# Performance work log

Hardware: AMD Instinct MI355X
Metric: run time of the kernel (lower is better)

The kernel has to match this reference:

```python
import jax, jax.numpy as jnp
import numpy as np

HEADS = 8
DIM_HEAD = 64
DIM = 512
HIDDEN = HEADS * DIM_HEAD  # 512


def setup_inputs() -> dict:
    key = jax.random.key(0)
    k1, k2, k3, k4 = jax.random.split(key, 4)
    B, H, W = 8, 64, 64
    x = jax.random.normal(k1, (B, DIM, H, W), dtype=jnp.float32)
    # Conv2d 1x1 weights stored as [out_ch, in_ch] (kernel 1x1 squeezed)
    w_qkv = jax.random.normal(k2, (3 * HIDDEN, DIM), dtype=jnp.float32) * (1.0 / np.sqrt(DIM))
    w_out = jax.random.normal(k3, (DIM, HIDDEN), dtype=jnp.float32) * (1.0 / np.sqrt(HIDDEN))
    b_out = jax.random.normal(k4, (DIM,), dtype=jnp.float32) * 0.01
    return {"x": x, "w_qkv": w_qkv, "w_out": w_out, "b_out": b_out}


def reference(x, w_qkv, w_out, b_out):
    b, c, h, w = x.shape
    n = h * w
    # to_qkv: 1x1 conv == channel GEMM
    qkv = jnp.einsum('bchw,oc->bohw', x, w_qkv)               # [b, 3*heads*dh, h, w]
    qkv = qkv.reshape(b, 3, HEADS, DIM_HEAD, n)               # split (qkv heads c), flatten (h w)
    q, k, v = qkv[:, 0], qkv[:, 1], qkv[:, 2]                 # each [b, heads, dh, n]
    k = jax.nn.softmax(k, axis=-1)                            # softmax over spatial tokens
    context = jnp.einsum('bhdn,bhen->bhde', k, v)             # [b, heads, dh, dh]
    out = jnp.einsum('bhde,bhdn->bhen', context, q)           # [b, heads, dh, n]
    out = out.reshape(b, HIDDEN, h, w)
    # to_out: 1x1 conv with bias
    return jnp.einsum('bchw,oc->bohw', out, w_out) + b_out[None, :, None, None]
```

## Files before the change

kernel.cpp:

```cpp
#include <hip/hip_runtime.h>
#include <hip/hip_bf16.h>


typedef __attribute__((ext_vector_type(8))) __bf16 bf16x8;
typedef __attribute__((ext_vector_type(4))) float f32x4;
typedef __attribute__((ext_vector_type(8))) unsigned short u16x8;

__device__ __forceinline__ unsigned short f2b(float f) {
  unsigned int u = __builtin_bit_cast(unsigned int, f);
  unsigned int r = (u + 0x7FFFu + ((u >> 16) & 1u)) >> 16;
  return (unsigned short)r;
}
__device__ __forceinline__ float b2f(unsigned short h) {
  unsigned int u = ((unsigned int)h) << 16;
  return __builtin_bit_cast(float, u);
}

__global__ __launch_bounds__(256) void prep_wkv_kernel(const float* __restrict__ w,
                                                       unsigned short* __restrict__ wkv) {
  int i = (blockIdx.x * 256 + threadIdx.x) * 4;
  const float* src = w + 512 * 512;
  #pragma unroll
  for (int j = 0; j < 4; ++j) wkv[i + j] = f2b(src[i + j]);
}

__global__ __launch_bounds__(256) void prep_wqT_kernel(const float* __restrict__ w,
                                                       unsigned short* __restrict__ WqT) {
  __shared__ unsigned short tile[64][65];
  const int ct = blockIdx.x, ot = blockIdx.y;
  const int c0 = ct * 64, o0 = ot * 64;
  const int tc = threadIdx.x & 63, tr = threadIdx.x >> 6;
  #pragma unroll
  for (int i = 0; i < 16; ++i) {
    int row = tr * 16 + i;
    tile[tc][row] = f2b(w[(long)(o0 + row) * 512 + c0 + tc]);
  }
  __syncthreads();
  #pragma unroll
  for (int i = 0; i < 16; ++i) {
    int row = tr * 16 + i;
    WqT[(long)(c0 + row) * 512 + o0 + tc] = tile[row][tc];
  }
}

__global__ __launch_bounds__(256) void transpose_x_kernel(const float* __restrict__ x,
                                                          unsigned short* __restrict__ xT) {
  __shared__ unsigned short tile[64][65];
  const int b = blockIdx.z, ct = blockIdx.y, nt = blockIdx.x;
  const int c0 = ct * 64, n0 = nt * 64;
  const int tc = threadIdx.x & 63, tr = threadIdx.x >> 6;
  const float* xp = x + ((long)b * 512 + c0) * 4096 + n0;
  #pragma unroll
  for (int i = 0; i < 16; ++i) {
    int row = tr * 16 + i;
    tile[tc][row] = f2b(xp[(long)row * 4096 + tc]);
  }
  __syncthreads();
  unsigned short* xtp = xT + ((long)b * 4096 + n0) * 512 + c0;
  #pragma unroll
  for (int i = 0; i < 16; ++i) {
    int row = tr * 16 + i;
    xtp[(long)row * 512 + tc] = tile[row][tc];
  }
}

__global__ __launch_bounds__(256) void gemm128_bt(
    const unsigned short* __restrict__ A, long strideA,
    const unsigned short* __restrict__ BT, long strideBT,
    void* __restrict__ Cout, long strideC, int ldc,
    const float* __restrict__ bias) {
  constexpr int K = 512;
  const int b = blockIdx.z;
  const int m0 = blockIdx.y * 128;
  const int n0 = blockIdx.x * 128;
  const unsigned short* Ab = A + (long)b * strideA;
  const unsigned short* Bb = BT + (long)b * strideBT;

  __shared__ unsigned short lds[2 * 128 * 64];
  char* ldsc = (char*)lds;

  const int tid = threadIdx.x;
  const int wave = tid >> 6;
  const int lane = tid & 63;
  const int wr = wave >> 1;
  const int wc = wave & 1;

  f32x4 acc[4][4];
  const f32x4 zero = {0.f, 0.f, 0.f, 0.f};
  #pragma unroll
  for (int i = 0; i < 4; ++i)
    #pragma unroll
    for (int j = 0; j < 4; ++j) acc[i][j] = zero;

  for (int kt = 0; kt < K; kt += 64) {
    #pragma unroll
    for (int q = 0; q < 4; ++q) {
      unsigned base = q * 4096 + wave * 1024;
      unsigned D = base + lane * 16;
      unsigned row = D >> 7;
      unsigned g = (D >> 4) & 7;
      unsigned gl = g ^ (row & 7);
      const unsigned short* srcA = Ab + (long)(m0 + row) * K + kt + gl * 8;
      __builtin_amdgcn_global_load_lds(
          (const __attribute__((address_space(1))) unsigned int*)srcA,
          (__attribute__((address_space(3))) unsigned int*)(ldsc + base), 16, 0, 0);
      const unsigned short* srcB = Bb + (long)(n0 + row) * K + kt + gl * 8;
      __builtin_amdgcn_global_load_lds(
          (const __attribute__((address_space(1))) unsigned int*)srcB,
          (__attribute__((address_space(3))) unsigned int*)(ldsc + 16384 + base), 16, 0, 0);
    }
    __syncthreads();

    bf16x8 af[2][4], bfr[2][4];
    #pragma unroll
    for (int ks = 0; ks < 2; ++ks) {
      #pragma unroll
      for (int mi = 0; mi < 4; ++mi) {
        unsigned row = wr * 64 + mi * 16 + (lane & 15);
        unsigned g = ((unsigned)(ks * 4 + (lane >> 4))) ^ (row & 7);
        af[ks][mi] = *(const bf16x8*)(ldsc + row * 128 + g * 16);
      }
      #pragma unroll
      for (int ni = 0; ni < 4; ++ni) {
        unsigned row = wc * 64 + ni * 16 + (lane & 15);
        unsigned g = ((unsigned)(ks * 4 + (lane >> 4))) ^ (row & 7);
        bfr[ks][ni] = *(const bf16x8*)(ldsc + 16384 + row * 128 + g * 16);
      }
    }
    #pragma unroll
    for (int ks = 0; ks < 2; ++ks)
      #pragma unroll
      for (int mi = 0; mi < 4; ++mi)
        #pragma unroll
        for (int ni = 0; ni < 4; ++ni)
          acc[mi][ni] = __builtin_amdgcn_mfma_f32_16x16x32_bf16(
              af[ks][mi], bfr[ks][ni], acc[mi][ni], 0, 0, 0);
    __syncthreads();
  }

  const int r0 = (lane >> 4) * 4;
  const int cn = lane & 15;
  if (bias != nullptr) {
    float* C = (float*)Cout + (long)b * strideC;
    #pragma unroll
    for (int mi = 0; mi < 4; ++mi) {
      int o = m0 + wr * 64 + mi * 16 + r0;
      #pragma unroll
      for (int ni = 0; ni < 4; ++ni) {
        int n = n0 + wc * 64 + ni * 16 + cn;
        #pragma unroll
        for (int r = 0; r < 4; ++r)
          C[(long)(o + r) * ldc + n] = acc[mi][ni][r] + bias[o + r];
      }
    }
  } else {
    unsigned short* C = (unsigned short*)Cout + (long)b * strideC;
    #pragma unroll
    for (int mi = 0; mi < 4; ++mi) {
      int o = m0 + wr * 64 + mi * 16 + r0;
      #pragma unroll
      for (int ni = 0; ni < 4; ++ni) {
        int n = n0 + wc * 64 + ni * 16 + cn;
        #pragma unroll
        for (int r = 0; r < 4; ++r)
          C[(long)(o + r) * ldc + n] = f2b(acc[mi][ni][r]);
      }
    }
  }
}

__global__ __launch_bounds__(256) void rowstat_kernel(const unsigned short* __restrict__ kv,
                                                      float* __restrict__ stats) {
  const int row = blockIdx.x;
  const int b = row >> 9, d = row & 511;
  const unsigned short* kp = kv + ((long)b * 1024 + d) * 4096;
  const int tid = threadIdx.x, wave = tid >> 6, lane = tid & 63;
  __shared__ float red[8];

  float v[16];
  u16x8 l0 = *(const u16x8*)(kp + tid * 8);
  u16x8 l1 = *(const u16x8*)(kp + 2048 + tid * 8);
  #pragma unroll
  for (int j = 0; j < 8; ++j) { v[j] = b2f(l0[j]); v[8 + j] = b2f(l1[j]); }

  float m = v[0];
  #pragma unroll
  for (int j = 1; j < 16; ++j) m = fmaxf(m, v[j]);
  #pragma unroll
  for (int off = 32; off > 0; off >>= 1) m = fmaxf(m, __shfl_xor(m, off));
  if (lane == 0) red[wave] = m;
  __syncthreads();
  m = fmaxf(fmaxf(red[0], red[1]), fmaxf(red[2], red[3]));

  float s = 0.f;
  #pragma unroll
  for (int j = 0; j < 16; ++j) s += __expf(v[j] - m);
  #pragma unroll
  for (int off = 32; off > 0; off >>= 1) s += __shfl_xor(s, off);
  if (lane == 0) red[4 + wave] = s;
  __syncthreads();
  if (tid == 0) {
    s = red[4] + red[5] + red[6] + red[7];
    stats[2 * row] = m;
    stats[2 * row + 1] = 1.0f / s;
  }
}

__global__ __launch_bounds__(256) void context_kernel(const unsigned short* __restrict__ kv,
                                                      const float* __restrict__ stats,
                                                      float* __restrict__ ctx_part) {
  const int s = blockIdx.x, bh = blockIdx.y, b = bh >> 3, h = bh & 7;
  const unsigned short* Kp = kv + ((long)b * 1024 + h * 64) * 4096;
  const unsigned short* Vp = kv + ((long)b * 1024 + 512 + h * 64) * 4096;
  const float* sb = stats + ((long)b * 512 + h * 64) * 2;
  const int tid = threadIdx.x, wave = tid >> 6, lane = tid & 63;

  float mrow[4], srow[4];
  #pragma unroll
  for (int mi = 0; mi < 4; ++mi) {
    int rA = mi * 16 + (lane & 15);
    mrow[mi] = sb[2 * rA];
    srow[mi] = sb[2 * rA + 1];
  }

  f32x4 acc[4][4];
  const f32x4 zero = {0.f, 0.f, 0.f, 0.f};
  #pragma unroll
  for (int i = 0; i < 4; ++i)
    #pragma unroll
    for (int j = 0; j < 4; ++j) acc[i][j] = zero;

  const int kbeg = s * 512 + wave * 128;
  for (int k0 = kbeg; k0 < kbeg + 128; k0 += 32) {
    const int kc = k0 + (lane >> 4) * 8;
    bf16x8 a[4], bv[4];
    #pragma unroll
    for (int mi = 0; mi < 4; ++mi) {
      u16x8 kr = *(const u16x8*)(Kp + (long)(mi * 16 + (lane & 15)) * 4096 + kc);
      u16x8 pr;
      #pragma unroll
      for (int j = 0; j < 8; ++j)
        pr[j] = f2b(__expf(b2f(kr[j]) - mrow[mi]) * srow[mi]);
      a[mi] = __builtin_bit_cast(bf16x8, pr);
    }
    #pragma unroll
    for (int ni = 0; ni < 4; ++ni)
      bv[ni] = *(const bf16x8*)(Vp + (long)(ni * 16 + (lane & 15)) * 4096 + kc);
    #pragma unroll
    for (int mi = 0; mi < 4; ++mi)
      #pragma unroll
      for (int ni = 0; ni < 4; ++ni)
        acc[mi][ni] = __builtin_amdgcn_mfma_f32_16x16x32_bf16(a[mi], bv[ni], acc[mi][ni], 0, 0, 0);
  }

  __shared__ float part[4][64][64];
  #pragma unroll
  for (int mi = 0; mi < 4; ++mi)
    #pragma unroll
    for (int ni = 0; ni < 4; ++ni)
      #pragma unroll
      for (int r = 0; r < 4; ++r)
        part[wave][mi * 16 + (lane >> 4) * 4 + r][ni * 16 + (lane & 15)] = acc[mi][ni][r];
  __syncthreads();
  float* cp = ctx_part + ((long)(s * 64 + bh)) * 4096;
  for (int i = tid; i < 4096; i += 256) {
    int dd = i >> 6, ee = i & 63;
    cp[i] = part[0][dd][ee] + part[1][dd][ee] + part[2][dd][ee] + part[3][dd][ee];
  }
}

__global__ __launch_bounds__(256) void w2_kernel(const float* __restrict__ ctx_part,
                                                 const float* __restrict__ w_out,
                                                 unsigned short* __restrict__ W2) {
  const int cq = blockIdx.x, bh = blockIdx.y, b = bh >> 3, h = bh & 7;
  __shared__ float cs[64][65];
  const int tid = threadIdx.x;
  for (int i = tid; i < 4096; i += 256) {
    float v = 0.f;
    #pragma unroll
    for (int s = 0; s < 8; ++s) v += ctx_part[((long)(s * 64 + bh)) * 4096 + i];
    cs[i >> 6][i & 63] = v;
  }
  __syncthreads();
  const int c = cq * 128 + (tid & 127);
  const int dbeg = (tid >> 7) * 32;
  const float* wp = w_out + (long)c * 512 + h * 64;
  float wrow[64];
  #pragma unroll
  for (int e = 0; e < 64; ++e) wrow[e] = wp[e];
  unsigned short* W2p = W2 + ((long)b * 512 + c) * 512 + h * 64;
  for (int dd = dbeg; dd < dbeg + 32; ++dd) {
    float s = 0.f;
    #pragma unroll
    for (int e = 0; e < 64; ++e) s = fmaf(wrow[e], cs[dd][e], s);
    W2p[dd] = f2b(s);
  }
}

extern "C" void kernel_launch(void* const* d_in, const int* in_sizes, int n_in,
                              void* d_out, int out_size, void* d_ws, size_t ws_size,
                              hipStream_t stream) {
  const float* x     = (const float*)d_in[0];
  const float* w_qkv = (const float*)d_in[1];
  const float* w_out = (const float*)d_in[2];
  const float* b_out = (const float*)d_in[3];

  char* ws = (char*)d_ws;
  unsigned short* xT   = (unsigned short*)ws;
  unsigned short* kv   = (unsigned short*)(ws + 33554432);
  unsigned short* wkv  = (unsigned short*)(ws + 100663296);
  unsigned short* WqT  = (unsigned short*)(ws + 101711872);
  float*          stats= (float*)(ws + 102236160);
  float*          ctxp = (float*)(ws + 102268928);
  unsigned short* W2   = (unsigned short*)(ws + 110657536);
  unsigned short* W3   = (unsigned short*)(ws + 114851840);

  prep_wkv_kernel<<<dim3(512), dim3(256), 0, stream>>>(w_qkv, wkv);
  prep_wqT_kernel<<<dim3(8, 8), dim3(256), 0, stream>>>(w_qkv, WqT);
  transpose_x_kernel<<<dim3(64, 8, 8), dim3(256), 0, stream>>>(x, xT);
  gemm128_bt<<<dim3(32, 8, 8), dim3(256), 0, stream>>>(
      wkv, 0L, xT, (long)4096 * 512, (void*)kv, (long)1024 * 4096, 4096, (const float*)nullptr);
  rowstat_kernel<<<dim3(4096), dim3(256), 0, stream>>>(kv, stats);
  context_kernel<<<dim3(8, 64), dim3(256), 0, stream>>>(kv, stats, ctxp);
  w2_kernel<<<dim3(4, 64), dim3(256), 0, stream>>>(ctxp, w_out, W2);
  gemm128_bt<<<dim3(4, 4, 8), dim3(256), 0, stream>>>(
      W2, (long)512 * 512, WqT, 0L, (void*)W3, (long)512 * 512, 512, (const float*)nullptr);
  gemm128_bt<<<dim3(32, 4, 8), dim3(256), 0, stream>>>(
      W3, (long)512 * 512, xT, (long)4096 * 512, d_out, (long)512 * 4096, 4096, b_out);
}
```

Measured before the change: 166.3 us.

## Double-buffer B tile in LDS and load A fragments directly from global

The GEMM kernel's main loop now stages only the B tile through LDS, using two buffers so the next K-slice is prefetched while the current one feeds the MFMAs. A fragments are read straight from global memory into registers instead of going through LDS. This is meant to overlap global loads with compute and halve LDS traffic. The cost is uncoalesced, uncached-by-LDS global reads of A by every wave (both wc waves reread the same rows), and a full vmcnt(0) wait each iteration that also waits on the prefetch.

```diff
diff --git a/kernel.cpp b/kernel.cpp
--- a/kernel.cpp
+++ b/kernel.cpp
@@ -85,6 +85,24 @@
   const int wr = wave >> 1;
   const int wc = wave & 1;
 
+  const unsigned drow = (unsigned)(wave * 8 + (lane >> 3));
+  const unsigned g0 = (unsigned)(lane & 7);
+
+#define STAGE_B(buf, kt)                                                              \
+  do {                                                                                \
+    _Pragma("unroll")                                                                 \
+    for (int q = 0; q < 4; ++q) {                                                     \
+      unsigned row_ = q * 32 + drow;                                                  \
+      unsigned gl_ = g0 ^ (row_ & 7);                                                 \
+      const unsigned short* srcB_ = Bb + (long)(n0 + row_) * K + (kt) + gl_ * 8;      \
+      __builtin_amdgcn_global_load_lds(                                               \
+          (const __attribute__((address_space(1))) unsigned int*)srcB_,               \
+          (__attribute__((address_space(3))) unsigned int*)(ldsc + (buf) * 16384 +    \
+                                                            q * 4096 + wave * 1024),  \
+          16, 0, 0);                                                                  \
+    }                                                                                 \
+  } while (0)
+
   f32x4 acc[4][4];
   const f32x4 zero = {0.f, 0.f, 0.f, 0.f};
   #pragma unroll
@@ -92,41 +110,35 @@
     #pragma unroll
     for (int j = 0; j < 4; ++j) acc[i][j] = zero;
 
+  STAGE_B(0, 0);
+  asm volatile("s_waitcnt vmcnt(0)" ::: "memory");
+  __syncthreads();
+  __builtin_amdgcn_sched_barrier(0);
+
+  #pragma unroll
   for (int kt = 0; kt < K; kt += 64) {
-    #pragma unroll
-    for (int q = 0; q < 4; ++q) {
-      unsigned base = q * 4096 + wave * 1024;
-      unsigned D = base + lane * 16;
-      unsigned row = D >> 7;
-      unsigned g = (D >> 4) & 7;
-      unsigned gl = g ^ (row & 7);
-      const unsigned short* srcA = Ab + (long)(m0 + row) * K + kt + gl * 8;
-      __builtin_amdgcn_global_load_lds(
-          (const __attribute__((address_space(1))) unsigned int*)srcA,
-          (__attribute__((address_space(3))) unsigned int*)(ldsc + base), 16, 0, 0);
-      const unsigned short* srcB = Bb + (long)(n0 + row) * K + kt + gl * 8;
-      __builtin_amdgcn_global_load_lds(
-          (const __attribute__((address_space(1))) unsigned int*)srcB,
-          (__attribute__((address_space(3))) unsigned int*)(ldsc + 16384 + base), 16, 0, 0);
-    }
-    __syncthreads();
-
-    bf16x8 af[2][4], bfr[2][4];
-    #pragma unroll
-    for (int ks = 0; ks < 2; ++ks) {
+    const int cur = (kt >> 6) & 1;
+
+    if (kt + 64 < K) STAGE_B(cur ^ 1, kt + 64);
+
+    bf16x8 af[2][4];
+    #pragma unroll
+    for (int ks = 0; ks < 2; ++ks)
       #pragma unroll
       for (int mi = 0; mi < 4; ++mi) {
-        unsigned row = wr * 64 + mi * 16 + (lane & 15);
-        unsigned g = ((unsigned)(ks * 4 + (lane >> 4))) ^ (row & 7);
-        af[ks][mi] = *(const bf16x8*)(ldsc + row * 128 + g * 16);
+        int row = m0 + wr * 64 + mi * 16 + (lane & 15);
+        af[ks][mi] = *(const bf16x8*)(Ab + (long)row * K + kt + ks * 32 + (lane >> 4) * 8);
       }
+
+    bf16x8 bfr[2][4];
+    #pragma unroll
+    for (int ks = 0; ks < 2; ++ks)
       #pragma unroll
       for (int ni = 0; ni < 4; ++ni) {
         unsigned row = wc * 64 + ni * 16 + (lane & 15);
         unsigned g = ((unsigned)(ks * 4 + (lane >> 4))) ^ (row & 7);
-        bfr[ks][ni] = *(const bf16x8*)(ldsc + 16384 + row * 128 + g * 16);
+        bfr[ks][ni] = *(const bf16x8*)(ldsc + cur * 16384 + row * 128 + g * 16);
       }
-    }
     #pragma unroll
     for (int ks = 0; ks < 2; ++ks)
       #pragma unroll
@@ -135,8 +147,12 @@
         for (int ni = 0; ni < 4; ++ni)
           acc[mi][ni] = __builtin_amdgcn_mfma_f32_16x16x32_bf16(
               af[ks][mi], bfr[ks][ni], acc[mi][ni], 0, 0, 0);
+
+    asm volatile("s_waitcnt vmcnt(0)" ::: "memory");
     __syncthreads();
-  }
+    __builtin_amdgcn_sched_barrier(0);
+  }
+#undef STAGE_B
 
   const int r0 = (lane >> 4) * 4;
   const int cn = lane & 15;
```

Result: slower. 225.9 us (+35.8%).

## Load GEMM MFMA fragments directly from global memory instead of staging through LDS

Applied to the files above, without the earlier changes.

The 128x128 GEMM kernel no longer stages A and B tiles into swizzled shared memory with global_load_lds and barriers. Each wave now reads its bf16x8 MFMA fragments straight from global memory, and the K loop is fully unrolled. This removes LDS traffic and the two syncthreads per K step. In exchange, every tile row is fetched separately by the two waves that share it, so global/L2 traffic doubles, and the loads are 16-byte strided per lane with weaker coalescing.

```diff
diff --git a/kernel.cpp b/kernel.cpp
--- a/kernel.cpp
+++ b/kernel.cpp
@@ -73,11 +73,6 @@
   const int b = blockIdx.z;
   const int m0 = blockIdx.y * 128;
   const int n0 = blockIdx.x * 128;
-  const unsigned short* Ab = A + (long)b * strideA;
-  const unsigned short* Bb = BT + (long)b * strideBT;
-
-  __shared__ unsigned short lds[2 * 128 * 64];
-  char* ldsc = (char*)lds;
 
   const int tid = threadIdx.x;
   const int wave = tid >> 6;
@@ -85,6 +80,11 @@
   const int wr = wave >> 1;
   const int wc = wave & 1;
 
+  const unsigned short* Arow = A + (long)b * strideA +
+                               (long)(m0 + wr * 64 + (lane & 15)) * K + (lane >> 4) * 8;
+  const unsigned short* Brow = BT + (long)b * strideBT +
+                               (long)(n0 + wc * 64 + (lane & 15)) * K + (lane >> 4) * 8;
+
   f32x4 acc[4][4];
   const f32x4 zero = {0.f, 0.f, 0.f, 0.f};
   #pragma unroll
@@ -92,41 +92,19 @@
     #pragma unroll
     for (int j = 0; j < 4; ++j) acc[i][j] = zero;
 
+  #pragma unroll
   for (int kt = 0; kt < K; kt += 64) {
-    #pragma unroll
-    for (int q = 0; q < 4; ++q) {
-      unsigned base = q * 4096 + wave * 1024;
-      unsigned D = base + lane * 16;
-      unsigned row = D >> 7;
-      unsigned g = (D >> 4) & 7;
-      unsigned gl = g ^ (row & 7);
-      const unsigned short* srcA = Ab + (long)(m0 + row) * K + kt + gl * 8;
-      __builtin_amdgcn_global_load_lds(
-          (const __attribute__((address_space(1))) unsigned int*)srcA,
-          (__attribute__((address_space(3))) unsigned int*)(ldsc + base), 16, 0, 0);
-      const unsigned short* srcB = Bb + (long)(n0 + row) * K + kt + gl * 8;
-      __builtin_amdgcn_global_load_lds(
-          (const __attribute__((address_space(1))) unsigned int*)srcB,
-          (__attribute__((address_space(3))) unsigned int*)(ldsc + 16384 + base), 16, 0, 0);
-    }
-    __syncthreads();
-
     bf16x8 af[2][4], bfr[2][4];
     #pragma unroll
-    for (int ks = 0; ks < 2; ++ks) {
-      #pragma unroll
-      for (int mi = 0; mi < 4; ++mi) {
-        unsigned row = wr * 64 + mi * 16 + (lane & 15);
-        unsigned g = ((unsigned)(ks * 4 + (lane >> 4))) ^ (row & 7);
-        af[ks][mi] = *(const bf16x8*)(ldsc + row * 128 + g * 16);
-      }
-      #pragma unroll
-      for (int ni = 0; ni < 4; ++ni) {
-        unsigned row = wc * 64 + ni * 16 + (lane & 15);
-        unsigned g = ((unsigned)(ks * 4 + (lane >> 4))) ^ (row & 7);
-        bfr[ks][ni] = *(const bf16x8*)(ldsc + 16384 + row * 128 + g * 16);
-      }
-    }
+    for (int ks = 0; ks < 2; ++ks)
+      #pragma unroll
+      for (int mi = 0; mi < 4; ++mi)
+        af[ks][mi] = *(const bf16x8*)(Arow + (long)(mi * 16) * K + kt + ks * 32);
+    #pragma unroll
+    for (int ks = 0; ks < 2; ++ks)
+      #pragma unroll
+      for (int ni = 0; ni < 4; ++ni)
+        bfr[ks][ni] = *(const bf16x8*)(Brow + (long)(ni * 16) * K + kt + ks * 32);
     #pragma unroll
     for (int ks = 0; ks < 2; ++ks)
       #pragma unroll
@@ -135,7 +113,6 @@
         for (int ni = 0; ni < 4; ++ni)
           acc[mi][ni] = __builtin_amdgcn_mfma_f32_16x16x32_bf16(
               af[ks][mi], bfr[ks][ni], acc[mi][ni], 0, 0, 0);
-    __syncthreads();
   }
 
   const int r0 = (lane >> 4) * 4;
```

After: 290.3 us. +74.6%, slower.
